# Kernel tuning notes

Measured on AMD Instinct MI355X. Metric: run time of the kernel, lower is better.

The kernel has to match this reference:

```python
import jax, jax.numpy as jnp
import numpy as np

N, E, FD, H, NG, LAT = 20000, 320000, 64, 4, 64, 512


def _gat(x, W, a_src, a_dst, b, src, dst):
    # x: [N, in]; W: [H*FD, in]; a_src/a_dst: [H, FD]; b: [H*FD]
    h = (x @ W.T).reshape(N, H, FD)
    s = jnp.sum(h * a_src, -1)   # [N, H]
    d = jnp.sum(h * a_dst, -1)   # [N, H]
    e = jax.nn.leaky_relu(s[src] + d[dst], negative_slope=0.2)  # [E', H]
    m = jax.ops.segment_max(e, dst, num_segments=N)
    ex = jnp.exp(e - m[dst])
    den = jax.ops.segment_sum(ex, dst, num_segments=N)
    alpha = ex / den[dst]                                        # [E', H]
    out = jax.ops.segment_sum(alpha[:, :, None] * h[src], dst, num_segments=N)
    return out.reshape(N, H * FD) + b


def setup_inputs() -> dict:
    key = jax.random.key(0)
    ks = jax.random.split(key, 24)
    inp = {}
    inp['street_feature'] = jax.random.normal(ks[0], (N, 128), jnp.float32)
    inp['building_feature'] = jax.random.normal(ks[1], (N, 5), jnp.float32)
    sm = jax.random.randint(ks[2], (N, 1), 0, 2).astype(jnp.float32)
    inp['street_mask'] = sm
    inp['building_mask'] = 1.0 - sm
    inp['edge_index'] = jax.random.randint(ks[3], (2, E), 0, N, dtype=jnp.int32)
    # batch: sorted graph ids covering all NG graphs (no empty segments)
    rest = jax.random.randint(ks[4], (N - NG,), 0, NG, dtype=jnp.int32)
    inp['batch'] = jnp.sort(jnp.concatenate([jnp.arange(NG, dtype=jnp.int32), rest]))

    def lin(k, o, i):
        s = 1.0 / np.sqrt(i)
        return jax.random.uniform(k, (o, i), jnp.float32, -s, s)

    inp['street_W'] = lin(ks[5], FD, 128); inp['street_b'] = jnp.zeros((FD,), jnp.float32)
    inp['building_W'] = lin(ks[6], FD, 5); inp['building_b'] = jnp.zeros((FD,), jnp.float32)
    inp['W1'] = lin(ks[7], H * FD, FD)
    inp['a_src1'] = jax.random.normal(ks[8], (H, FD), jnp.float32) * 0.1
    inp['a_dst1'] = jax.random.normal(ks[9], (H, FD), jnp.float32) * 0.1
    inp['b1'] = jnp.zeros((H * FD,), jnp.float32)
    inp['W2'] = lin(ks[10], H * FD, H * FD)
    inp['a_src2'] = jax.random.normal(ks[11], (H, FD), jnp.float32) * 0.1
    inp['a_dst2'] = jax.random.normal(ks[12], (H, FD), jnp.float32) * 0.1
    inp['b2'] = jnp.zeros((H * FD,), jnp.float32)
    inp['W3'] = lin(ks[13], H * FD, H * FD)
    inp['a_src3'] = jax.random.normal(ks[14], (H, FD), jnp.float32) * 0.1
    inp['a_dst3'] = jax.random.normal(ks[15], (H, FD), jnp.float32) * 0.1
    inp['b3'] = jnp.zeros((H * FD,), jnp.float32)
    agg_in = FD * (1 + H * 3)  # 832
    inp['agg_W'] = lin(ks[16], LAT, agg_in); inp['agg_b'] = jnp.zeros((LAT,), jnp.float32)
    inp['mu_W'] = lin(ks[17], LAT, LAT); inp['mu_b'] = jnp.zeros((LAT,), jnp.float32)
    inp['var_W'] = lin(ks[18], LAT, LAT); inp['var_b'] = jnp.zeros((LAT,), jnp.float32)
    return inp


def reference(street_feature, building_feature, street_mask, building_mask,
              edge_index, batch,
              street_W, street_b, building_W, building_b,
              W1, a_src1, a_dst1, b1, W2, a_src2, a_dst2, b2,
              W3, a_src3, a_dst3, b3, agg_W, agg_b, mu_W, mu_b, var_W, var_b):
    sf = jax.nn.relu(street_feature @ street_W.T + street_b)
    bf = jax.nn.relu(building_feature @ building_W.T + building_b)
    n0 = sf * street_mask + bf * building_mask  # [N, FD]
    # add self loops (PyG GATConv default)
    loop = jnp.arange(N, dtype=edge_index.dtype)
    src = jnp.concatenate([edge_index[0], loop])
    dst = jnp.concatenate([edge_index[1], loop])
    n1 = jax.nn.relu(_gat(n0, W1, a_src1, a_dst1, b1, src, dst))
    n2 = jax.nn.relu(_gat(n1, W2, a_src2, a_dst2, b2, src, dst))
    n3 = jax.nn.relu(_gat(n2, W3, a_src3, a_dst3, b3, src, dst))
    g0 = jax.ops.segment_max(n0, batch, num_segments=NG)
    g1 = jax.ops.segment_max(n1, batch, num_segments=NG)
    g2 = jax.ops.segment_max(n2, batch, num_segments=NG)
    g3 = jax.ops.segment_max(n3, batch, num_segments=NG)
    g = jnp.concatenate([g0, g1, g2, g3], axis=1)  # [NG, FD*(1+3H)]
    latent = g @ agg_W.T + agg_b
    mu = latent @ mu_W.T + mu_b
    log_var = latent @ var_W.T + var_b
    return (mu, log_var)
```

## Files before the change

### kernel.cpp

```cpp
#include <hip/hip_runtime.h>
#include <math.h>

#define NNODES 20000
#define NEDGES 320000
#define FDIM 64
#define NHEAD 4
#define NGR 64
#define LATD 512
#define HF 256
#define NEP (NEDGES + NNODES)
#define AGGIN 832
#define MPAD 20032

typedef float f32x4 __attribute__((ext_vector_type(4)));
typedef short bf16x8 __attribute__((ext_vector_type(8)));
typedef unsigned short u16x8 __attribute__((ext_vector_type(8)));

__device__ inline unsigned short f2bf(float f) {
    unsigned u = __float_as_uint(f);
    unsigned r = (u + 0x7FFF + ((u >> 16) & 1)) >> 16;
    return (unsigned short)r;
}
__device__ inline float bf2f(unsigned short h) {
    return __uint_as_float(((unsigned)h) << 16);
}
__device__ inline unsigned short f2h(float f) {
    _Float16 h = (_Float16)f;
    unsigned short u;
    __builtin_memcpy(&u, &h, 2);
    return u;
}
__device__ inline float h2f(unsigned short u) {
    _Float16 h;
    __builtin_memcpy(&h, &u, 2);
    return (float)h;
}

#define EDGE_BLOCKS4 ((NEP + 1023) / 1024)
#define CONV_N (HF * FDIM + 2 * HF * HF)
#define CONV_BLOCKS ((CONV_N + 255) / 256)
#define ENC_BLOCKS (NNODES / 32)
#define GEMM_BLOCKS (NNODES / 32)
#define SLAB_BLOCKS ((NNODES + 31) / 32)

__global__ void prep_kernel(
    const int* __restrict__ ei, int* __restrict__ cnt,
    const float* __restrict__ W1, const float* __restrict__ W2, const float* __restrict__ W3,
    unsigned short* __restrict__ W1hi, unsigned short* __restrict__ W1lo,
    unsigned short* __restrict__ W2hi, unsigned short* __restrict__ W2lo,
    unsigned short* __restrict__ W3hi, unsigned short* __restrict__ W3lo)
{
    if (blockIdx.x < EDGE_BLOCKS4) {
        int i0 = blockIdx.x * 1024 + threadIdx.x;
#pragma unroll
        for (int u = 0; u < 4; u++) {
            int i = i0 + u * 256;
            if (i < NEDGES) {
                atomicAdd(&cnt[ei[NEDGES + i]], 1);
            } else if (i < NEP) {
                atomicAdd(&cnt[i - NEDGES], 1);
            }
        }
    } else {
        int i = (blockIdx.x - EDGE_BLOCKS4) * 256 + threadIdx.x;
        const int n1 = HF * FDIM, n2 = HF * HF;
        const float* src; unsigned short *hi, *lo; int j;
        if (i < n1) { src = W1; hi = W1hi; lo = W1lo; j = i; }
        else if (i < n1 + n2) { src = W2; hi = W2hi; lo = W2lo; j = i - n1; }
        else if (i < n1 + 2 * n2) { src = W3; hi = W3hi; lo = W3lo; j = i - n1 - n2; }
        else return;
        float f = src[j];
        unsigned short h = f2bf(f);
        hi[j] = h;
        lo[j] = f2bf(f - bf2f(h));
    }
}

__global__ __launch_bounds__(1024) void scan_deg(const int* __restrict__ deg, int* __restrict__ offs)
{
    __shared__ int wt[16];
    const int per = (NNODES + 1023) / 1024;
    int t = threadIdx.x, lane = t & 63, w = t >> 6;
    int start = t * per;
    int end = start + per; if (end > NNODES) end = NNODES;
    int s = 0;
    for (int i = start; i < end; i++) s += deg[i];
    int pref = s;
#pragma unroll
    for (int m = 1; m < 64; m <<= 1) {
        int v = __shfl_up(pref, m, 64);
        if (lane >= m) pref += v;
    }
    if (lane == 63) wt[w] = pref;
    __syncthreads();
    int wadd = 0;
    for (int i = 0; i < w; i++) wadd += wt[i];
    int acc = wadd + pref - s;
    for (int i = start; i < end; i++) { offs[i] = acc; acc += deg[i]; }
    if (t == 1023) offs[NNODES] = NEP;
}

__global__ __launch_bounds__(256) void scatter_encode(
    const int* __restrict__ ei, const int* __restrict__ offs,
    int* __restrict__ cnt2, int* __restrict__ csr_src,
    const float* __restrict__ sfeat, const float* __restrict__ bfeat,
    const float* __restrict__ smask, const float* __restrict__ bmask,
    const float* __restrict__ sW, const float* __restrict__ sb,
    const float* __restrict__ bW, const float* __restrict__ bb,
    const int* __restrict__ batch,
    unsigned short* __restrict__ nhi, unsigned short* __restrict__ nlo,
    int* __restrict__ g)
{
    __shared__ float wlds[64 * 132];
    if (blockIdx.x < EDGE_BLOCKS4) {
        int i0 = blockIdx.x * 1024 + threadIdx.x;
        int sv[4], dv[4];
#pragma unroll
        for (int u = 0; u < 4; u++) {
            int i = i0 + u * 256;
            if (i < NEDGES) { sv[u] = ei[i]; dv[u] = ei[NEDGES + i]; }
            else if (i < NEP) { sv[u] = i - NEDGES; dv[u] = i - NEDGES; }
            else { sv[u] = -1; dv[u] = 0; }
        }
#pragma unroll
        for (int u = 0; u < 4; u++) {
            if (sv[u] >= 0) {
                int p = offs[dv[u]] + atomicAdd(&cnt2[dv[u]], 1);
                csr_src[p] = sv[u];
            }
        }
        return;
    }
    int bid = blockIdx.x - EDGE_BLOCKS4;
    int t = threadIdx.x;
#pragma unroll
    for (int it = 0; it < 8; it++) {
        int idx = it * 256 + t;
        int f = idx >> 5, k4 = idx & 31;
        float4 v = *(const float4*)(sW + f * 128 + k4 * 4);
        *(float4*)(&wlds[f * 132 + k4 * 4]) = v;
    }
    __syncthreads();

    int lane = t & 63, wave = t >> 6;
    int nb = bid * 32 + wave * 8;

    float acc[8];
#pragma unroll
    for (int i = 0; i < 8; i++) acc[i] = 0.f;

    const float* xbase = sfeat + (size_t)nb * 128;
    for (int k4 = 0; k4 < 32; k4++) {
        float4 wv = *(const float4*)(&wlds[lane * 132 + k4 * 4]);
#pragma unroll
        for (int i = 0; i < 8; i++) {
            float4 xv = *(const float4*)(xbase + i * 128 + k4 * 4);
            acc[i] += xv.x * wv.x + xv.y * wv.y + xv.z * wv.z + xv.w * wv.w;
        }
    }

    float bwr[5];
#pragma unroll
    for (int k = 0; k < 5; k++) bwr[k] = bW[lane * 5 + k];
    float sbv = sb[lane], bbv = bb[lane];

    int curb = batch[nb];
    float m = 0.f;
#pragma unroll
    for (int i = 0; i < 8; i++) {
        int node = nb + i;
        float accb = 0.f;
#pragma unroll
        for (int k = 0; k < 5; k++) accb += bfeat[node * 5 + k] * bwr[k];
        float sv = fmaxf(acc[i] + sbv, 0.f);
        float bv = fmaxf(accb + bbv, 0.f);
        float val = sv * smask[node] + bv * bmask[node];
        unsigned short hb = f2bf(val);
        nhi[(size_t)node * FDIM + lane] = hb;
        nlo[(size_t)node * FDIM + lane] = f2bf(val - bf2f(hb));
        int b = batch[node];
        if (b != curb) {
            atomicMax(&g[curb * AGGIN + lane], __float_as_int(m));
            m = 0.f; curb = b;
        }
        m = fmaxf(m, val);
    }
    atomicMax(&g[curb * AGGIN + lane], __float_as_int(m));
}

template <int K>
__global__ __launch_bounds__(256) void gemm_attn_mfma(
    const unsigned short* __restrict__ xhi, const unsigned short* __restrict__ xlo,
    const unsigned short* __restrict__ Whi, const unsigned short* __restrict__ Wlo,
    const float* __restrict__ a_src, const float* __restrict__ a_dst,
    unsigned short* __restrict__ h, float* __restrict__ s, float* __restrict__ d,
    const int* __restrict__ batch, int* __restrict__ g, int slabcol)
{
    if (blockIdx.x >= GEMM_BLOCKS) {
        int f = threadIdx.x;
        int r0 = (blockIdx.x - GEMM_BLOCKS) * 32;
        if (r0 >= NNODES) return;
        int r1 = r0 + 32; if (r1 > NNODES) r1 = NNODES;
        int cur = batch[r0];
        float m = 0.f;
        for (int r = r0; r < r1; r++) {
            int b = batch[r];
            if (b != cur) {
                atomicMax(&g[cur * AGGIN + slabcol + f], __float_as_int(m));
                m = 0.f; cur = b;
            }
            size_t idx = (size_t)r * HF + f;
            float val = bf2f(xhi[idx]) + bf2f(xlo[idx]);
            m = fmaxf(m, val);
        }
        atomicMax(&g[cur * AGGIN + slabcol + f], __float_as_int(m));
        return;
    }

    int t = threadIdx.x, lane = t & 63, w = t >> 6;
    int colid = lane & 15, quad = lane >> 4;
    int nb = blockIdx.x * 32;

    f32x4 acc[2][4];
#pragma unroll
    for (int mt = 0; mt < 2; mt++)
#pragma unroll
        for (int nt = 0; nt < 4; nt++)
#pragma unroll
            for (int r = 0; r < 4; r++) acc[mt][nt][r] = 0.f;

    for (int kc = 0; kc < K; kc += 32) {
        bf16x8 bhi[4], blo[4], ahi[2], alo[2];
#pragma unroll
        for (int nt = 0; nt < 4; nt++) {
            size_t boff = (size_t)(w * 64 + nt * 16 + colid) * K + kc + quad * 8;
            bhi[nt] = *(const bf16x8*)&Whi[boff];
            blo[nt] = *(const bf16x8*)&Wlo[boff];
        }
#pragma unroll
        for (int mt = 0; mt < 2; mt++) {
            size_t aoff = (size_t)(nb + mt * 16 + colid) * K + kc + quad * 8;
            ahi[mt] = *(const bf16x8*)&xhi[aoff];
            alo[mt] = *(const bf16x8*)&xlo[aoff];
        }
#pragma unroll
        for (int mt = 0; mt < 2; mt++)
#pragma unroll
            for (int nt = 0; nt < 4; nt++) {
                acc[mt][nt] = __builtin_amdgcn_mfma_f32_16x16x32_bf16(ahi[mt], bhi[nt], acc[mt][nt], 0, 0, 0);
                acc[mt][nt] = __builtin_amdgcn_mfma_f32_16x16x32_bf16(ahi[mt], blo[nt], acc[mt][nt], 0, 0, 0);
                acc[mt][nt] = __builtin_amdgcn_mfma_f32_16x16x32_bf16(alo[mt], bhi[nt], acc[mt][nt], 0, 0, 0);
            }
    }

#pragma unroll
    for (int mt = 0; mt < 2; mt++) {
#pragma unroll
        for (int r = 0; r < 4; r++) {
            int node = nb + mt * 16 + quad * 4 + r;
#pragma unroll
            for (int nt = 0; nt < 4; nt++)
                h[(size_t)node * HF + w * 64 + nt * 16 + colid] = f2h(acc[mt][nt][r]);
        }
    }

    float as_r[4], ad_r[4];
#pragma unroll
    for (int nt = 0; nt < 4; nt++) {
        as_r[nt] = a_src[w * 64 + nt * 16 + colid];
        ad_r[nt] = a_dst[w * 64 + nt * 16 + colid];
    }
#pragma unroll
    for (int mt = 0; mt < 2; mt++) {
#pragma unroll
        for (int r = 0; r < 4; r++) {
            float ps = 0.f, pd = 0.f;
#pragma unroll
            for (int nt = 0; nt < 4; nt++) {
                ps += acc[mt][nt][r] * as_r[nt];
                pd += acc[mt][nt][r] * ad_r[nt];
            }
#pragma unroll
            for (int m = 1; m < 16; m <<= 1) {
                ps += __shfl_xor(ps, m, 64);
                pd += __shfl_xor(pd, m, 64);
            }
            if (colid == 0) {
                int node = nb + mt * 16 + quad * 4 + r;
                s[(size_t)node * NHEAD + w] = ps;
                d[(size_t)node * NHEAD + w] = pd;
            }
        }
    }
}

__global__ __launch_bounds__(256) void gat_aggr(
    const unsigned short* __restrict__ h, const float* __restrict__ s, const float* __restrict__ d,
    const int* __restrict__ offs, const int* __restrict__ csr_src,
    const float* __restrict__ bias,
    unsigned short* __restrict__ ohi, unsigned short* __restrict__ olo)
{
    int t = threadIdx.x;
    int lane = t & 63;
    int wv = t >> 6;
    int node = blockIdx.x * 4 + wv;
    int eh = lane >> 5;
    int p = lane & 31;
    int hd2 = p >> 3;
    int f0 = p * 8;
    int lo = offs[node], hi = offs[node + 1];
    int deg = hi - lo;

    float a[8];
#pragma unroll
    for (int j = 0; j < 8; j++) a[j] = 0.f;
    float inv;

    if (deg <= 64) {
        int slot = lane >> 2, hd = lane & 3;
        float dn = d[(size_t)node * NHEAD + hd];
        float ev[4];
        int sv[4];
#pragma unroll
        for (int c = 0; c < 4; c++) {
            int k = c * 16 + slot;
            float e = -3.402823466e38f;
            int src = 0;
            if (k < deg) {
                src = csr_src[lo + k];
                float ee = s[(size_t)src * NHEAD + hd] + dn;
                e = fmaxf(ee, 0.2f * ee);
            }
            ev[c] = e; sv[c] = src;
        }
        float mx = fmaxf(fmaxf(ev[0], ev[1]), fmaxf(ev[2], ev[3]));
#pragma unroll
        for (int m = 4; m < 64; m <<= 1) mx = fmaxf(mx, __shfl_xor(mx, m, 64));
        float den = 0.f;
#pragma unroll
        for (int c = 0; c < 4; c++) {
            ev[c] = __expf(ev[c] - mx);
            den += ev[c];
        }
#pragma unroll
        for (int m = 4; m < 64; m <<= 1) den += __shfl_xor(den, m, 64);

        inv = 1.f / __shfl(den, hd2);

#pragma unroll
        for (int c = 0; c < 4; c++) {
            int base = c * 16;
            if (base >= deg) break;
            int n16 = deg - base; if (n16 > 16) n16 = 16;
            for (int kk = 0; kk < n16; kk += 8) {
                float ex[4]; int sr[4]; u16x8 hv[4];
#pragma unroll
                for (int u = 0; u < 4; u++) {
                    int sl = (kk + u * 2 + eh) * 4 + hd2;
                    ex[u] = __shfl(ev[c], sl);
                    sr[u] = __shfl(sv[c], sl);
                }
#pragma unroll
                for (int u = 0; u < 4; u++)
                    hv[u] = *(const u16x8*)(h + (size_t)sr[u] * HF + f0);
#pragma unroll
                for (int u = 0; u < 4; u++)
#pragma unroll
                    for (int j = 0; j < 8; j++) a[j] += ex[u] * h2f(hv[u][j]);
            }
        }
    } else {
        float dn2 = d[(size_t)node * NHEAD + hd2];
        float mx = -3.402823466e38f;
        for (int i = lo; i < hi; i++) {
            int src = csr_src[i];
            float e = s[(size_t)src * NHEAD + hd2] + dn2;
            e = fmaxf(e, 0.2f * e);
            mx = fmaxf(mx, e);
        }
        float den = 0.f;
        for (int i = lo + eh; i < hi; i += 2) {
            int src = csr_src[i];
            float e = s[(size_t)src * NHEAD + hd2] + dn2;
            e = fmaxf(e, 0.2f * e);
            float ex = __expf(e - mx);
            den += ex;
            u16x8 hv = *(const u16x8*)(h + (size_t)src * HF + f0);
#pragma unroll
            for (int j = 0; j < 8; j++) a[j] += ex * h2f(hv[j]);
        }
        den += __shfl_xor(den, 32, 64);
        inv = 1.f / den;
    }

#pragma unroll
    for (int j = 0; j < 8; j++) a[j] += __shfl_xor(a[j], 32, 64);

    if (eh == 0) {
        float v[8];
#pragma unroll
        for (int j = 0; j < 8; j++) v[j] = fmaxf(a[j] * inv + bias[f0 + j], 0.f);
        ushort4 hb0, lb0, hb1, lb1;
        hb0.x = f2bf(v[0]); lb0.x = f2bf(v[0] - bf2f(hb0.x));
        hb0.y = f2bf(v[1]); lb0.y = f2bf(v[1] - bf2f(hb0.y));
        hb0.z = f2bf(v[2]); lb0.z = f2bf(v[2] - bf2f(hb0.z));
        hb0.w = f2bf(v[3]); lb0.w = f2bf(v[3] - bf2f(hb0.w));
        hb1.x = f2bf(v[4]); lb1.x = f2bf(v[4] - bf2f(hb1.x));
        hb1.y = f2bf(v[5]); lb1.y = f2bf(v[5] - bf2f(hb1.y));
        hb1.z = f2bf(v[6]); lb1.z = f2bf(v[6] - bf2f(hb1.z));
        hb1.w = f2bf(v[7]); lb1.w = f2bf(v[7] - bf2f(hb1.w));
        *(ushort4*)(ohi + (size_t)node * HF + f0) = hb0;
        *(ushort4*)(ohi + (size_t)node * HF + f0 + 4) = hb1;
        *(ushort4*)(olo + (size_t)node * HF + f0) = lb0;
        *(ushort4*)(olo + (size_t)node * HF + f0 + 4) = lb1;
    }
}

__global__ __launch_bounds__(256) void seg_max_slab_bf(
    const unsigned short* __restrict__ xhi, const unsigned short* __restrict__ xlo,
    const int* __restrict__ batch, int* __restrict__ g, int coloff)
{
    int f = threadIdx.x;
    int r0 = blockIdx.x * 32;
    if (r0 >= NNODES) return;
    int r1 = r0 + 32; if (r1 > NNODES) r1 = NNODES;
    int cur = batch[r0];
    float m = 0.f;
    for (int r = r0; r < r1; r++) {
        int b = batch[r];
        if (b != cur) {
            atomicMax(&g[cur * AGGIN + coloff + f], __float_as_int(m));
            m = 0.f; cur = b;
        }
        size_t idx = (size_t)r * HF + f;
        float val = bf2f(xhi[idx]) + bf2f(xlo[idx]);
        m = fmaxf(m, val);
    }
    atomicMax(&g[cur * AGGIN + coloff + f], __float_as_int(m));
}

__global__ __launch_bounds__(256) void mlp_latent(
    const float* __restrict__ g, const float* __restrict__ W, const float* __restrict__ b,
    float* __restrict__ latent)
{
    int idx = blockIdx.x * 256 + threadIdx.x;
    int r = idx >> 9, c = idx & 511;
    const float4* gv = (const float4*)(g + (size_t)r * AGGIN);
    const float4* wv = (const float4*)(W + (size_t)c * AGGIN);
    float acc = 0.f;
#pragma unroll 4
    for (int k = 0; k < AGGIN / 4; k++) {
        float4 a = gv[k], w = wv[k];
        acc += a.x * w.x + a.y * w.y + a.z * w.z + a.w * w.w;
    }
    latent[idx] = acc + b[c];
}

__global__ __launch_bounds__(256) void mlp_head(
    const float* __restrict__ latent,
    const float* __restrict__ muW, const float* __restrict__ mub,
    const float* __restrict__ vW, const float* __restrict__ vb,
    float* __restrict__ out)
{
    int idx = blockIdx.x * 256 + threadIdx.x;
    int half = idx >> 15;
    int j = idx & 32767;
    int r = j >> 9, c = j & 511;
    const float* W = half ? vW : muW;
    const float* bb = half ? vb : mub;
    const float4* lv = (const float4*)(latent + (size_t)r * LATD);
    const float4* wv = (const float4*)(W + (size_t)c * LATD);
    float acc = 0.f;
#pragma unroll 4
    for (int k = 0; k < LATD / 4; k++) {
        float4 a = lv[k], w = wv[k];
        acc += a.x * w.x + a.y * w.y + a.z * w.z + a.w * w.w;
    }
    out[idx] = acc + bb[c];
}

static inline size_t align16(size_t x) { return (x + 15) & ~(size_t)15; }

extern "C" void kernel_launch(void* const* d_in, const int* in_sizes, int n_in,
                              void* d_out, int out_size, void* d_ws, size_t ws_size,
                              hipStream_t stream)
{
    const float* sfeat = (const float*)d_in[0];
    const float* bfeat = (const float*)d_in[1];
    const float* smask = (const float*)d_in[2];
    const float* bmask = (const float*)d_in[3];
    const int*   ei    = (const int*)d_in[4];
    const int*   batch = (const int*)d_in[5];
    const float* sW = (const float*)d_in[6];
    const float* sb = (const float*)d_in[7];
    const float* bW = (const float*)d_in[8];
    const float* bb = (const float*)d_in[9];
    const float* W1 = (const float*)d_in[10];
    const float* as1 = (const float*)d_in[11];
    const float* ad1 = (const float*)d_in[12];
    const float* b1 = (const float*)d_in[13];
    const float* W2 = (const float*)d_in[14];
    const float* as2 = (const float*)d_in[15];
    const float* ad2 = (const float*)d_in[16];
    const float* b2 = (const float*)d_in[17];
    const float* W3 = (const float*)d_in[18];
    const float* as3 = (const float*)d_in[19];
    const float* ad3 = (const float*)d_in[20];
    const float* b3 = (const float*)d_in[21];
    const float* aggW = (const float*)d_in[22];
    const float* aggb = (const float*)d_in[23];
    const float* muW = (const float*)d_in[24];
    const float* mub = (const float*)d_in[25];
    const float* vW = (const float*)d_in[26];
    const float* vb = (const float*)d_in[27];
    float* out = (float*)d_out;

    char* ws = (char*)d_ws;
    size_t off = 0;
    unsigned short* h = (unsigned short*)(ws + off); off = align16(off + (size_t)NNODES * HF * 2);
    unsigned short* Ahi = (unsigned short*)(ws + off); off = align16(off + (size_t)MPAD * HF * 2);
    unsigned short* Alo = (unsigned short*)(ws + off); off = align16(off + (size_t)MPAD * HF * 2);
    float* s  = (float*)(ws + off); off = align16(off + (size_t)NNODES * NHEAD * 4);
    float* d  = (float*)(ws + off); off = align16(off + (size_t)NNODES * NHEAD * 4);
    int* offs = (int*)(ws + off);   off = align16(off + (size_t)(NNODES + 1) * 4);
    size_t zstart = off;
    int* cnt  = (int*)(ws + off);   off = align16(off + (size_t)NNODES * 4);
    int* cnt2 = (int*)(ws + off);   off = align16(off + (size_t)NNODES * 4);
    float* g  = (float*)(ws + off); off = align16(off + (size_t)NGR * AGGIN * 4);
    size_t zbytes = off - zstart;
    int* csr  = (int*)(ws + off);   off = align16(off + (size_t)NEP * 4);
    float* lat = (float*)(ws + off); off = align16(off + (size_t)NGR * LATD * 4);
    unsigned short* W1hi = (unsigned short*)(ws + off); off = align16(off + (size_t)HF * FDIM * 2);
    unsigned short* W1lo = (unsigned short*)(ws + off); off = align16(off + (size_t)HF * FDIM * 2);
    unsigned short* W2hi = (unsigned short*)(ws + off); off = align16(off + (size_t)HF * HF * 2);
    unsigned short* W2lo = (unsigned short*)(ws + off); off = align16(off + (size_t)HF * HF * 2);
    unsigned short* W3hi = (unsigned short*)(ws + off); off = align16(off + (size_t)HF * HF * 2);
    unsigned short* W3lo = (unsigned short*)(ws + off); off = align16(off + (size_t)HF * HF * 2);

    hipMemsetAsync(ws + zstart, 0, zbytes, stream);

    prep_kernel<<<EDGE_BLOCKS4 + CONV_BLOCKS, 256, 0, stream>>>(
        ei, cnt, W1, W2, W3, W1hi, W1lo, W2hi, W2lo, W3hi, W3lo);
    scan_deg<<<1, 1024, 0, stream>>>(cnt, offs);
    scatter_encode<<<EDGE_BLOCKS4 + ENC_BLOCKS, 256, 0, stream>>>(
        ei, offs, cnt2, csr,
        sfeat, bfeat, smask, bmask, sW, sb, bW, bb, batch, Ahi, Alo, (int*)g);

    gemm_attn_mfma<FDIM><<<GEMM_BLOCKS, 256, 0, stream>>>(
        Ahi, Alo, W1hi, W1lo, as1, ad1, h, s, d, batch, (int*)g, -1);
    gat_aggr<<<NNODES / 4, 256, 0, stream>>>(h, s, d, offs, csr, b1, Ahi, Alo);

    gemm_attn_mfma<HF><<<GEMM_BLOCKS + SLAB_BLOCKS, 256, 0, stream>>>(
        Ahi, Alo, W2hi, W2lo, as2, ad2, h, s, d, batch, (int*)g, FDIM);
    gat_aggr<<<NNODES / 4, 256, 0, stream>>>(h, s, d, offs, csr, b2, Ahi, Alo);

    gemm_attn_mfma<HF><<<GEMM_BLOCKS + SLAB_BLOCKS, 256, 0, stream>>>(
        Ahi, Alo, W3hi, W3lo, as3, ad3, h, s, d, batch, (int*)g, FDIM + HF);
    gat_aggr<<<NNODES / 4, 256, 0, stream>>>(h, s, d, offs, csr, b3, Ahi, Alo);

    seg_max_slab_bf<<<SLAB_BLOCKS, 256, 0, stream>>>(Ahi, Alo, batch, (int*)g, FDIM + 2 * HF);

    mlp_latent<<<(NGR * LATD + 255) / 256, 256, 0, stream>>>(g, aggW, aggb, lat);
    mlp_head<<<(2 * NGR * LATD + 255) / 256, 256, 0, stream>>>(lat, muW, mub, vW, vb, out);
}
```

Baseline: 430.1 us.

## Double-buffer GEMM operand loads and split segment-max out of GEMM kernel

The MFMA GEMM K-loop now prefetches the next 32-wide chunk of bf16 hi/lo operands into a second register buffer, fully unrolled, so global loads overlap the MFMA work. The per-graph segment-max slab blocks that rode along in the GEMM launches move out into separate seg_max_slab_bf launches after each aggregation. Launch bounds also request 3 blocks per SIMD. The cost is two extra kernel launches and higher register pressure from the double buffers, which the occupancy hint may push into spills.

```diff
diff --git a/kernel.cpp b/kernel.cpp
--- a/kernel.cpp
+++ b/kernel.cpp
@@ -189,34 +189,13 @@
 }
 
 template <int K>
-__global__ __launch_bounds__(256) void gemm_attn_mfma(
+__global__ __launch_bounds__(256, 3) void gemm_attn_mfma(
     const unsigned short* __restrict__ xhi, const unsigned short* __restrict__ xlo,
     const unsigned short* __restrict__ Whi, const unsigned short* __restrict__ Wlo,
     const float* __restrict__ a_src, const float* __restrict__ a_dst,
-    unsigned short* __restrict__ h, float* __restrict__ s, float* __restrict__ d,
-    const int* __restrict__ batch, int* __restrict__ g, int slabcol)
-{
-    if (blockIdx.x >= GEMM_BLOCKS) {
-        int f = threadIdx.x;
-        int r0 = (blockIdx.x - GEMM_BLOCKS) * 32;
-        if (r0 >= NNODES) return;
-        int r1 = r0 + 32; if (r1 > NNODES) r1 = NNODES;
-        int cur = batch[r0];
-        float m = 0.f;
-        for (int r = r0; r < r1; r++) {
-            int b = batch[r];
-            if (b != cur) {
-                atomicMax(&g[cur * AGGIN + slabcol + f], __float_as_int(m));
-                m = 0.f; cur = b;
-            }
-            size_t idx = (size_t)r * HF + f;
-            float val = bf2f(xhi[idx]) + bf2f(xlo[idx]);
-            m = fmaxf(m, val);
-        }
-        atomicMax(&g[cur * AGGIN + slabcol + f], __float_as_int(m));
-        return;
-    }
-
+    unsigned short* __restrict__ h, float* __restrict__ s, float* __restrict__ d)
+{
+    constexpr int NCHUNK = K / 32;
     int t = threadIdx.x, lane = t & 63, w = t >> 6;
     int colid = lane & 15, quad = lane >> 4;
     int nb = blockIdx.x * 32;
@@ -229,27 +208,35 @@
 #pragma unroll
             for (int r = 0; r < 4; r++) acc[mt][nt][r] = 0.f;
 
-    for (int kc = 0; kc < K; kc += 32) {
-        bf16x8 bhi[4], blo[4], ahi[2], alo[2];
+    bf16x8 bhi[2][4], blo[2][4], ahi[2][2], alo[2][2];
+
+    auto load_chunk = [&](int kc, int buf) {
 #pragma unroll
         for (int nt = 0; nt < 4; nt++) {
             size_t boff = (size_t)(w * 64 + nt * 16 + colid) * K + kc + quad * 8;
-            bhi[nt] = *(const bf16x8*)&Whi[boff];
-            blo[nt] = *(const bf16x8*)&Wlo[boff];
+            bhi[buf][nt] = *(const bf16x8*)&Whi[boff];
+            blo[buf][nt] = *(const bf16x8*)&Wlo[boff];
         }
 #pragma unroll
         for (int mt = 0; mt < 2; mt++) {
             size_t aoff = (size_t)(nb + mt * 16 + colid) * K + kc + quad * 8;
-            ahi[mt] = *(const bf16x8*)&xhi[aoff];
-            alo[mt] = *(const bf16x8*)&xlo[aoff];
-        }
+            ahi[buf][mt] = *(const bf16x8*)&xhi[aoff];
+            alo[buf][mt] = *(const bf16x8*)&xlo[aoff];
+        }
+    };
+
+    load_chunk(0, 0);
+#pragma unroll
+    for (int c = 0; c < NCHUNK; c++) {
+        int buf = c & 1;
+        if (c + 1 < NCHUNK) load_chunk((c + 1) * 32, buf ^ 1);
 #pragma unroll
         for (int mt = 0; mt < 2; mt++)
 #pragma unroll
             for (int nt = 0; nt < 4; nt++) {
-                acc[mt][nt] = __builtin_amdgcn_mfma_f32_16x16x32_bf16(ahi[mt], bhi[nt], acc[mt][nt], 0, 0, 0);
-                acc[mt][nt] = __builtin_amdgcn_mfma_f32_16x16x32_bf16(ahi[mt], blo[nt], acc[mt][nt], 0, 0, 0);
-                acc[mt][nt] = __builtin_amdgcn_mfma_f32_16x16x32_bf16(alo[mt], bhi[nt], acc[mt][nt], 0, 0, 0);
+                acc[mt][nt] = __builtin_amdgcn_mfma_f32_16x16x32_bf16(ahi[buf][mt], bhi[buf][nt], acc[mt][nt], 0, 0, 0);
+                acc[mt][nt] = __builtin_amdgcn_mfma_f32_16x16x32_bf16(ahi[buf][mt], blo[buf][nt], acc[mt][nt], 0, 0, 0);
+                acc[mt][nt] = __builtin_amdgcn_mfma_f32_16x16x32_bf16(alo[buf][mt], bhi[buf][nt], acc[mt][nt], 0, 0, 0);
             }
     }
 
@@ -547,17 +534,18 @@
         sfeat, bfeat, smask, bmask, sW, sb, bW, bb, batch, Ahi, Alo, (int*)g);
 
     gemm_attn_mfma<FDIM><<<GEMM_BLOCKS, 256, 0, stream>>>(
-        Ahi, Alo, W1hi, W1lo, as1, ad1, h, s, d, batch, (int*)g, -1);
+        Ahi, Alo, W1hi, W1lo, as1, ad1, h, s, d);
     gat_aggr<<<NNODES / 4, 256, 0, stream>>>(h, s, d, offs, csr, b1, Ahi, Alo);
-
-    gemm_attn_mfma<HF><<<GEMM_BLOCKS + SLAB_BLOCKS, 256, 0, stream>>>(
-        Ahi, Alo, W2hi, W2lo, as2, ad2, h, s, d, batch, (int*)g, FDIM);
+    seg_max_slab_bf<<<SLAB_BLOCKS, 256, 0, stream>>>(Ahi, Alo, batch, (int*)g, FDIM);
+
+    gemm_attn_mfma<HF><<<GEMM_BLOCKS, 256, 0, stream>>>(
+        Ahi, Alo, W2hi, W2lo, as2, ad2, h, s, d);
     gat_aggr<<<NNODES / 4, 256, 0, stream>>>(h, s, d, offs, csr, b2, Ahi, Alo);
-
-    gemm_attn_mfma<HF><<<GEMM_BLOCKS + SLAB_BLOCKS, 256, 0, stream>>>(
-        Ahi, Alo, W3hi, W3lo, as3, ad3, h, s, d, batch, (int*)g, FDIM + HF);
+    seg_max_slab_bf<<<SLAB_BLOCKS, 256, 0, stream>>>(Ahi, Alo, batch, (int*)g, FDIM + HF);
+
+    gemm_attn_mfma<HF><<<GEMM_BLOCKS, 256, 0, stream>>>(
+        Ahi, Alo, W3hi, W3lo, as3, ad3, h, s, d);
     gat_aggr<<<NNODES / 4, 256, 0, stream>>>(h, s, d, offs, csr, b3, Ahi, Alo);
-
     seg_max_slab_bf<<<SLAB_BLOCKS, 256, 0, stream>>>(Ahi, Alo, batch, (int*)g, FDIM + 2 * HF);
 
     mlp_latent<<<(NGR * LATD + 255) / 256, 256, 0, stream>>>(g, aggW, aggb, lat);
```

New measurement: 442.1 us. 1.03x slower.
